# Performance work log

Hardware: AMD Instinct MI355X
Metric: run time of the kernel (lower is better)

## Reference

```python
import jax, jax.numpy as jnp
import numpy as np
import math

B, D, TX, TY = 16, 192, 512, 2048
NEG = -1e9


def _neg_cent(x_mean, x_logs, z):
    # x_mean, x_logs: [B, D, TX]; z: [B, D, TY] -> neg_cent: [B, TY, TX]
    s_p_sq_r = jnp.exp(-2.0 * x_logs)                                   # [B,D,TX]
    nc1 = jnp.sum(-0.5 * math.log(2.0 * math.pi) - x_logs, axis=1, keepdims=True)  # [B,1,TX]
    nc2 = jnp.einsum('bdy,bdx->byx', -0.5 * z * z, s_p_sq_r)            # [B,TY,TX]
    nc3 = jnp.einsum('bdy,bdx->byx', z, x_mean * s_p_sq_r)              # [B,TY,TX]
    nc4 = jnp.sum(-0.5 * x_mean * x_mean * s_p_sq_r, axis=1, keepdims=True)  # [B,1,TX]
    return nc1 + nc2 + nc3 + nc4


def _mas_single(nc):
    # Monotonic alignment search (Viterbi DP) for one sample. nc: [TY, TX]
    ty, tx = nc.shape
    xs = jnp.arange(tx)

    def fwd_step(v_prev, inp):
        nc_row, y = inp
        v_diag = jnp.concatenate([jnp.full((1,), NEG, nc.dtype), v_prev[:-1]])
        take_diag = v_diag > v_prev                                      # bool [TX]
        v = nc_row + jnp.maximum(v_prev, v_diag)
        v = jnp.where(xs <= y, v, NEG)                                   # path cannot be ahead of time
        return v, take_diag

    v0 = jnp.where(xs == 0, nc[0], NEG)
    _, dirs = jax.lax.scan(fwd_step, v0, (nc[1:], jnp.arange(1, ty)))    # dirs: [TY-1, TX]

    def bwd_step(idx, d_row):
        # idx = path position at row y; move to y-1
        new_idx = idx - d_row[idx].astype(idx.dtype)
        return new_idx, idx

    idx0, path_tail = jax.lax.scan(bwd_step, jnp.array(tx - 1, jnp.int32), dirs, reverse=True)
    path = jnp.concatenate([idx0[None], path_tail])                      # [TY]
    return jax.nn.one_hot(path, tx, dtype=nc.dtype)                      # [TY, TX]


def _forward(x_mean, x_logs, z, logw):
    neg_cent = jax.lax.stop_gradient(_neg_cent(x_mean, x_logs, z))
    attn = jax.lax.stop_gradient(jax.vmap(_mas_single)(neg_cent))        # [B,TY,TX]
    w = jnp.sum(attn, axis=1, keepdims=True)                             # [B,1,TX] durations
    logw_ = jnp.log(w + 1e-6)
    l_length = jnp.sum((logw - logw_) ** 2, axis=(1, 2))                 # [B]
    m_p = jnp.einsum('byx,bdx->bdy', attn, x_mean)                       # [B,D,TY]
    logs_p = jnp.einsum('byx,bdx->bdy', attn, x_logs)                    # [B,D,TY]
    out_main = jnp.concatenate([m_p, logs_p], axis=1)                    # [B,2D,TY]
    return out_main, l_length, attn


def setup_inputs() -> dict:
    key = jax.random.key(0)
    k1, k2, k3, k4 = jax.random.split(key, 4)
    return {
        'x_mean': jax.random.normal(k1, (B, D, TX), jnp.float32),
        'x_logs': jax.random.normal(k2, (B, D, TX), jnp.float32),
        'z': jax.random.normal(k3, (B, D, TY), jnp.float32),
        'logw': jax.random.normal(k4, (B, 1, TX), jnp.float32),
    }


def reference(x_mean, x_logs, z, logw):
    return _forward(x_mean, x_logs, z, logw)
```

## Files before the change

kernel.cpp:

```cpp
#include <hip/hip_runtime.h>
#include <hip/hip_bf16.h>
#include <math.h>

#define B_   16
#define D_   192
#define TX_  512
#define TY_  2048
#define NEGV (-1e9f)



typedef __attribute__((address_space(1))) const float glob_f;
typedef __attribute__((address_space(3))) float       lds_f;

__global__ __launch_bounds__(512) void precomp(const float* __restrict__ xm,
                                               const float* __restrict__ xl,
                                               float* __restrict__ S,
                                               float* __restrict__ MS,
                                               float* __restrict__ Cpart) {
    int b = blockIdx.x;
    int p = blockIdx.y;
    int x = threadIdx.x;
    size_t base = ((size_t)b * D_ + p * 32) * TX_;
    const float* mb = xm + base;
    const float* lb = xl + base;
    float* Sb  = S  + base;
    float* MSb = MS + base;
    float c = 0.f;
    for (int d = 0; d < 32; d++) {
        float lg = lb[d * TX_ + x];
        float mn = mb[d * TX_ + x];
        float s  = expf(-2.f * lg);
        float ms = mn * s;
        Sb[d * TX_ + x]  = s;
        MSb[d * TX_ + x] = ms;
        c += -0.9189385332046727f - lg - 0.5f * mn * mn * s;
    }
    Cpart[(b * 6 + p) * TX_ + x] = c;
}

__global__ __launch_bounds__(256) void gemm_nc(const float* __restrict__ z,
                                               const float* __restrict__ S,
                                               const float* __restrict__ MS,
                                               const float* __restrict__ Cpart,
                                               float* __restrict__ NC) {
    int bx = blockIdx.x;
    int by = blockIdx.y;
    int b  = blockIdx.z;
    int tid = threadIdx.x;
    int tx = tid & 15, ty = tid >> 4;
    __shared__ __align__(16) float Zt[16 * 128];
    __shared__ __align__(16) float St[16 * 128];
    __shared__ __align__(16) float MSt[16 * 128];

    float acc[8][8];
#pragma unroll
    for (int i = 0; i < 8; i++)
#pragma unroll
        for (int j = 0; j < 8; j++) acc[i][j] = 0.f;

    int x0 = bx * 128, y0 = by * 128;
    const float* zb  = z  + (size_t)b * D_ * TY_;
    const float* Sb  = S  + (size_t)b * D_ * TX_;
    const float* MSb = MS + (size_t)b * D_ * TX_;

    for (int k0 = 0; k0 < D_; k0 += 16) {
#pragma unroll
        for (int j = 0; j < 2; j++) {
            int f = tid + j * 256;
            int kk = f >> 5, c = (f & 31) * 4;
            __builtin_amdgcn_global_load_lds((glob_f*)(zb  + (size_t)(k0 + kk) * TY_ + y0 + c),
                                             (lds_f*)(Zt  + f * 4), 16, 0, 0);
            __builtin_amdgcn_global_load_lds((glob_f*)(Sb  + (size_t)(k0 + kk) * TX_ + x0 + c),
                                             (lds_f*)(St  + f * 4), 16, 0, 0);
            __builtin_amdgcn_global_load_lds((glob_f*)(MSb + (size_t)(k0 + kk) * TX_ + x0 + c),
                                             (lds_f*)(MSt + f * 4), 16, 0, 0);
        }
        __syncthreads();

#pragma unroll 2
        for (int kk = 0; kk < 16; kk++) {
            float4 z0 = *(const float4*)&Zt[kk * 128 + ty * 4];
            float4 z1 = *(const float4*)&Zt[kk * 128 + 64 + ty * 4];
            float4 s0 = *(const float4*)&St[kk * 128 + tx * 4];
            float4 s1 = *(const float4*)&St[kk * 128 + 64 + tx * 4];
            float4 m0 = *(const float4*)&MSt[kk * 128 + tx * 4];
            float4 m1 = *(const float4*)&MSt[kk * 128 + 64 + tx * 4];
            float4 u0, u1;
            u0.x = -0.5f * z0.x * z0.x; u0.y = -0.5f * z0.y * z0.y;
            u0.z = -0.5f * z0.z * z0.z; u0.w = -0.5f * z0.w * z0.w;
            u1.x = -0.5f * z1.x * z1.x; u1.y = -0.5f * z1.y * z1.y;
            u1.z = -0.5f * z1.z * z1.z; u1.w = -0.5f * z1.w * z1.w;
            float zz[8] = {z0.x, z0.y, z0.z, z0.w, z1.x, z1.y, z1.z, z1.w};
            float uu[8] = {u0.x, u0.y, u0.z, u0.w, u1.x, u1.y, u1.z, u1.w};
            float ss[8] = {s0.x, s0.y, s0.z, s0.w, s1.x, s1.y, s1.z, s1.w};
            float mm[8] = {m0.x, m0.y, m0.z, m0.w, m1.x, m1.y, m1.z, m1.w};
#pragma unroll
            for (int i = 0; i < 8; i++)
#pragma unroll
                for (int j = 0; j < 8; j++)
                    acc[i][j] += uu[i] * ss[j] + zz[i] * mm[j];
        }
        __syncthreads();
    }

    float cv[8] = {0, 0, 0, 0, 0, 0, 0, 0};
#pragma unroll
    for (int p = 0; p < 6; p++) {
        float4 c0 = *(const float4*)&Cpart[(b * 6 + p) * TX_ + x0 + tx * 4];
        float4 c1 = *(const float4*)&Cpart[(b * 6 + p) * TX_ + x0 + 64 + tx * 4];
        cv[0] += c0.x; cv[1] += c0.y; cv[2] += c0.z; cv[3] += c0.w;
        cv[4] += c1.x; cv[5] += c1.y; cv[6] += c1.z; cv[7] += c1.w;
    }

#pragma unroll
    for (int i = 0; i < 8; i++) {
        int y = y0 + ty * 4 + (i & 3) + 64 * (i >> 2);
        float4 o0, o1;
        o0.x = acc[i][0] + cv[0]; o0.y = acc[i][1] + cv[1];
        o0.z = acc[i][2] + cv[2]; o0.w = acc[i][3] + cv[3];
        o1.x = acc[i][4] + cv[4]; o1.y = acc[i][5] + cv[5];
        o1.z = acc[i][6] + cv[6]; o1.w = acc[i][7] + cv[7];
        *(float4*)&NC[((size_t)b * TY_ + y) * TX_ + x0 + tx * 4]      = o0;
        *(float4*)&NC[((size_t)b * TY_ + y) * TX_ + x0 + 64 + tx * 4] = o1;
    }
}

__global__ __launch_bounds__(128, 1) void mas_forward(const float* __restrict__ NC,
                                                      unsigned char* __restrict__ dirs) {
    int b = blockIdx.x;
    int tid = threadIdx.x;
    int wave = tid >> 6;
    int lane = tid & 63;
    const float* ncb = NC + (size_t)b * TY_ * TX_;

    __shared__ __align__(16) float ring[64][512];
    __shared__ int prod_cnt;
    __shared__ int cons_cnt;
    if (tid == 0) { prod_cnt = 0; cons_cnt = 0; }
    __syncthreads();

    if (wave == 1) {
        for (int k = 0; k < 128; k++) {
            while (k - __hip_atomic_load(&cons_cnt, __ATOMIC_ACQUIRE,
                                         __HIP_MEMORY_SCOPE_WORKGROUP) >= 4)
                __builtin_amdgcn_s_sleep(1);
            int slot0 = (k & 3) * 16;
#pragma unroll
            for (int r = 0; r < 16; r++) {
                int y = 1 + k * 16 + r;
                if (y > 2047) y = 2047;
                const float* g = ncb + (size_t)y * TX_ + lane * 4;
                float* l = &ring[slot0 + r][0];
                __builtin_amdgcn_global_load_lds((glob_f*)g,         (lds_f*)l,         16, 0, 0);
                __builtin_amdgcn_global_load_lds((glob_f*)(g + 256), (lds_f*)(l + 256), 16, 0, 0);
            }
            asm volatile("s_waitcnt vmcnt(0)" ::: "memory");
            if (lane == 0)
                __hip_atomic_store(&prod_cnt, k + 1, __ATOMIC_RELEASE,
                                   __HIP_MEMORY_SCOPE_WORKGROUP);
        }
    } else {
        float v[8];
#pragma unroll
        for (int j = 0; j < 8; j++) v[j] = NEGV;
        if (lane == 0) v[0] = ncb[0];

        unsigned char* db = dirs + (size_t)b * 2048 * 64 + lane;
        float bound = NEGV;

        auto row_step = [&](float4 a, float4 c, int y, bool mask) {
            float ncv[8] = {a.x, a.y, a.z, a.w, c.x, c.y, c.z, c.w};
            float vd0 = (lane == 0) ? NEGV : bound;
            float v6o = v[6], v7o = v[7];
            float v7n = ncv[7] + fmaxf(v7o, v6o);
            if (mask && y < 511 && lane * 8 + 7 > y) v7n = NEGV;
            bound = __shfl_up(v7n, 1);
            unsigned bits = (v6o > v7o) ? 0x80u : 0u;
            float vd = vd0;
#pragma unroll
            for (int j = 0; j < 7; j++) {
                float vp = v[j];
                bits |= (vd > vp) ? (1u << j) : 0u;
                v[j] = ncv[j] + fmaxf(vp, vd);
                vd = vp;
            }
            if (mask && y < 511) {
                int xb = lane * 8;
#pragma unroll
                for (int j = 0; j < 7; j++)
                    if (xb + j > y) v[j] = NEGV;
            }
            v[7] = v7n;
            db[(size_t)(y - 1) * 64] = (unsigned char)bits;
        };

        auto wait_chunk = [&](int k) {
            while (__hip_atomic_load(&prod_cnt, __ATOMIC_ACQUIRE,
                                     __HIP_MEMORY_SCOPE_WORKGROUP) < k + 1)
                __builtin_amdgcn_s_sleep(1);
        };
        auto done_chunk = [&](int k) {
            if (lane == 0)
                __hip_atomic_store(&cons_cnt, k + 1, __ATOMIC_RELEASE,
                                   __HIP_MEMORY_SCOPE_WORKGROUP);
        };

        int y = 1;
        for (int k = 0; k < 32; k++) {
            wait_chunk(k);
            int slot0 = (k & 3) * 16;
#pragma unroll
            for (int r = 0; r < 16; r++) {
                float4 a = *(const float4*)&ring[slot0 + r][lane * 8];
                float4 c = *(const float4*)&ring[slot0 + r][lane * 8 + 4];
                row_step(a, c, y, true);
                y++;
            }
            done_chunk(k);
        }
        for (int k = 32; k < 127; k++) {
            wait_chunk(k);
            int slot0 = (k & 3) * 16;
#pragma unroll
            for (int r = 0; r < 16; r++) {
                float4 a = *(const float4*)&ring[slot0 + r][lane * 8];
                float4 c = *(const float4*)&ring[slot0 + r][lane * 8 + 4];
                row_step(a, c, y, false);
                y++;
            }
            done_chunk(k);
        }
        wait_chunk(127);
        {
            int slot0 = (127 & 3) * 16;
#pragma unroll
            for (int r = 0; r < 15; r++) {
                float4 a = *(const float4*)&ring[slot0 + r][lane * 8];
                float4 c = *(const float4*)&ring[slot0 + r][lane * 8 + 4];
                row_step(a, c, y, false);
                y++;
            }
            done_chunk(127);
        }
    }
}

__global__ __launch_bounds__(64, 1) void mas_backtrack(const unsigned* __restrict__ dirs,
                                                       int* __restrict__ path) {
    int b = blockIdx.x;
    int lane = threadIdx.x;
    const unsigned* db = dirs + (size_t)b * 2048 * 16;
    int idx = TX_ - 1;

    for (int y_hi = 2047; y_hi >= 1; y_hi -= 64) {
        int wb = (idx >> 5) - 2;
        if (wb < 0) wb = 0;
        int base = wb << 5;
        int y = y_hi - lane;
        unsigned w0 = 0, w1 = 0, w2 = 0;
        if (y >= 1) {
            const unsigned* r = db + (size_t)(y - 1) * 16 + wb;
            w0 = r[0]; w1 = r[1]; w2 = r[2];
        }
        int steps = (y_hi < 64) ? y_hi : 64;
        int my_path = 0;
#pragma unroll 8
        for (int t = 0; t < steps; t++) {
            if (lane == t) my_path = idx;
            unsigned u0 = (unsigned)__shfl((int)w0, t);
            unsigned u1 = (unsigned)__shfl((int)w1, t);
            unsigned u2 = (unsigned)__shfl((int)w2, t);
            int off = idx - base;
            unsigned w = (off < 32) ? u0 : ((off < 64) ? u1 : u2);
            idx -= (int)((w >> (off & 31)) & 1u);
        }
        if (lane < steps) path[b * TY_ + (y_hi - lane)] = my_path;
    }
    if (lane == 0) path[b * TY_ + 0] = idx;
}

__global__ __launch_bounds__(512) void durations_ll(const int* __restrict__ path,
                                                    const float* __restrict__ logw,
                                                    float* __restrict__ out_l) {
    int b = blockIdx.x;
    int tid = threadIdx.x;
    __shared__ int wcnt[TX_];
    __shared__ float partial[8];
    wcnt[tid] = 0;
    __syncthreads();
    for (int y = tid; y < TY_; y += 512)
        atomicAdd(&wcnt[path[b * TY_ + y]], 1);
    __syncthreads();
    float t = logw[b * TX_ + tid] - logf((float)wcnt[tid] + 1e-6f);
    float sq = t * t;
#pragma unroll
    for (int off = 32; off > 0; off >>= 1) sq += __shfl_down(sq, off);
    if ((tid & 63) == 0) partial[tid >> 6] = sq;
    __syncthreads();
    if (tid == 0) {
        float s = 0.f;
#pragma unroll
        for (int i = 0; i < 8; i++) s += partial[i];
        out_l[b] = s;
    }
}

__global__ __launch_bounds__(256) void gather_main(const int* __restrict__ path,
                                                   const float* __restrict__ xm,
                                                   const float* __restrict__ xl,
                                                   float* __restrict__ out) {
    int c = blockIdx.x;
    int b = blockIdx.y;
    int tid = threadIdx.x;
    const float* src = (c < D_) ? (xm + ((size_t)b * D_ + c) * TX_)
                                : (xl + ((size_t)b * D_ + (c - D_)) * TX_);
    const int* pb = path + b * TY_;
    float* ob = out + ((size_t)b * 2 * D_ + c) * TY_;
#pragma unroll
    for (int k = 0; k < 8; k++) {
        int y = tid + k * 256;
        ob[y] = src[pb[y]];
    }
}

__global__ __launch_bounds__(128) void write_attn(const int* __restrict__ path,
                                                  float* __restrict__ attn) {
    int blk = blockIdx.x;
    int b = blk >> 11;
    int y = blk & 2047;
    int tid = threadIdx.x;
    int p = path[b * TY_ + y];
    float4 val = make_float4(0.f, 0.f, 0.f, 0.f);
    if ((p >> 2) == tid) {
        int r = p & 3;
        if (r == 0) val.x = 1.f;
        else if (r == 1) val.y = 1.f;
        else if (r == 2) val.z = 1.f;
        else val.w = 1.f;
    }
    ((float4*)attn)[((size_t)blk) * 128 + tid] = val;
}

extern "C" void kernel_launch(void* const* d_in, const int* in_sizes, int n_in,
                              void* d_out, int out_size, void* d_ws, size_t ws_size,
                              hipStream_t stream) {
    const float* x_mean = (const float*)d_in[0];
    const float* x_logs = (const float*)d_in[1];
    const float* z      = (const float*)d_in[2];
    const float* logw   = (const float*)d_in[3];
    float* out = (float*)d_out;

    char* ws = (char*)d_ws;
    float* S            = (float*)(ws + 0);
    float* MS           = (float*)(ws + 6291456);
    float* NC           = (float*)(ws + 12615680);
    unsigned char* dirs = (unsigned char*)(ws + 79724544);
    float* Cpart        = (float*)(ws + 79724544);
    int* path           = (int*)(ws + 81821696);

    float* out_main = out;
    float* out_l    = out + 12582912;
    float* out_attn = out + 12582928;

    precomp<<<dim3(B_, 6), dim3(512), 0, stream>>>(x_mean, x_logs, S, MS, Cpart);
    gemm_nc<<<dim3(4, 16, 16), dim3(256), 0, stream>>>(z, S, MS, Cpart, NC);
    mas_forward<<<dim3(B_), dim3(128), 0, stream>>>(NC, dirs);
    mas_backtrack<<<dim3(B_), dim3(64), 0, stream>>>((const unsigned*)dirs, path);
    durations_ll<<<dim3(B_), dim3(512), 0, stream>>>(path, logw, out_l);
    gather_main<<<dim3(384, 16), dim3(256), 0, stream>>>(path, x_mean, x_logs, out_main);
    write_attn<<<dim3(B_ * TY_), dim3(128), 0, stream>>>(path, out_attn);
}
```

Baseline: 799.1 us.

## Split each lane's DP columns into two interleaved halves to shorten serial chain

In the Viterbi forward pass, each lane now owns two groups of 4 columns, one in the lower half of TX and one in the upper half, instead of 8 contiguous columns. The cross-lane boundary values for both halves come from a single rotated shuffle computed early, and lane 0's upper-half boundary is taken from lane 63's lower-half value. LDS reads become two conflict-free float4 loads per row. Direction bits are repacked with an xor-shuffle so each byte still covers 8 contiguous columns. The aim is to cut the serial dependency per row and let the shuffle overlap with the other column updates, at the cost of an extra shuffle and some bit-packing work.

```diff
diff --git a/kernel.cpp b/kernel.cpp
--- a/kernel.cpp
+++ b/kernel.cpp
@@ -166,33 +166,66 @@
         for (int j = 0; j < 8; j++) v[j] = NEGV;
         if (lane == 0) v[0] = ncb[0];
 
-        unsigned char* db = dirs + (size_t)b * 2048 * 64 + lane;
-        float bound = NEGV;
-
-        auto row_step = [&](float4 a, float4 c, int y, bool mask) {
-            float ncv[8] = {a.x, a.y, a.z, a.w, c.x, c.y, c.z, c.w};
-            float vd0 = (lane == 0) ? NEGV : bound;
-            float v6o = v[6], v7o = v[7];
-            float v7n = ncv[7] + fmaxf(v7o, v6o);
-            if (mask && y < 511 && lane * 8 + 7 > y) v7n = NEGV;
-            bound = __shfl_up(v7n, 1);
-            unsigned bits = (v6o > v7o) ? 0x80u : 0u;
-            float vd = vd0;
-#pragma unroll
-            for (int j = 0; j < 7; j++) {
-                float vp = v[j];
-                bits |= (vd > vp) ? (1u << j) : 0u;
-                v[j] = ncv[j] + fmaxf(vp, vd);
-                vd = vp;
-            }
-            if (mask && y < 511) {
-                int xb = lane * 8;
-#pragma unroll
-                for (int j = 0; j < 7; j++)
-                    if (xb + j > y) v[j] = NEGV;
-            }
-            v[7] = v7n;
-            db[(size_t)(y - 1) * 64] = (unsigned char)bits;
+        unsigned char* db = dirs + (size_t)b * 2048 * 64;
+        int doff = (lane & 1) ? (32 + (lane >> 1)) : (lane >> 1);
+        unsigned char* db2 = db + doff;
+
+        float boundA = NEGV;
+        float boundB = NEGV;
+        int lw = (lane + 63) & 63;
+
+        auto row_step = [&](float4 a, float4 c, int y, bool maskph) {
+            float vdA = (lane == 0) ? NEGV : boundA;
+            float vdB = boundB;
+            float o0 = v[0], o1 = v[1], o2 = v[2], o3 = v[3];
+            float o4 = v[4], o5 = v[5], o6 = v[6], o7 = v[7];
+            float n3 = a.w + fmaxf(o3, o2);
+            float n7 = c.w + fmaxf(o7, o6);
+            if (maskph) {
+                if (y < 255 && lane * 4 + 3 > y) n3 = NEGV;
+                if (y < 511 && lane * 4 + 259 > y) n7 = NEGV;
+            }
+            float sA = __shfl(n3, lw);
+            float sB = __shfl(n7, lw);
+            float n0 = a.x + fmaxf(o0, vdA);
+            float n1 = a.y + fmaxf(o1, o0);
+            float n2 = a.z + fmaxf(o2, o1);
+            float n4 = c.x + fmaxf(o4, vdB);
+            float n5 = c.y + fmaxf(o5, o4);
+            float n6 = c.z + fmaxf(o6, o5);
+            unsigned bits = 0;
+            bits |= (vdA > o0) ? 0x1u : 0u;
+            bits |= (o0 > o1) ? 0x2u : 0u;
+            bits |= (o1 > o2) ? 0x4u : 0u;
+            bits |= (o2 > o3) ? 0x8u : 0u;
+            bits |= (vdB > o4) ? 0x10u : 0u;
+            bits |= (o4 > o5) ? 0x20u : 0u;
+            bits |= (o5 > o6) ? 0x40u : 0u;
+            bits |= (o6 > o7) ? 0x80u : 0u;
+            if (maskph) {
+                int xa = lane * 4;
+                if (y < 255) {
+                    if (xa > y) n0 = NEGV;
+                    if (xa + 1 > y) n1 = NEGV;
+                    if (xa + 2 > y) n2 = NEGV;
+                }
+                int xb = 256 + lane * 4;
+                if (y < 511) {
+                    if (xb > y) n4 = NEGV;
+                    if (xb + 1 > y) n5 = NEGV;
+                    if (xb + 2 > y) n6 = NEGV;
+                }
+            }
+            v[0] = n0; v[1] = n1; v[2] = n2; v[3] = n3;
+            v[4] = n4; v[5] = n5; v[6] = n6; v[7] = n7;
+            boundA = sA;
+            boundB = (lane == 0) ? sA : sB;
+            unsigned pk = (bits & 0xFu) | ((bits & 0xF0u) << 4);
+            unsigned pr = (unsigned)__shfl_xor((int)pk, 1);
+            unsigned lowb  = (pk & 0xFu) | ((pr & 0xFu) << 4);
+            unsigned highb = ((pr >> 8) & 0xFu) | (((pk >> 8) & 0xFu) << 4);
+            unsigned byteval = (lane & 1) ? highb : lowb;
+            db2[(size_t)(y - 1) * 64] = (unsigned char)byteval;
         };
 
         auto wait_chunk = [&](int k) {
@@ -212,8 +245,8 @@
             int slot0 = (k & 3) * 16;
 #pragma unroll
             for (int r = 0; r < 16; r++) {
-                float4 a = *(const float4*)&ring[slot0 + r][lane * 8];
-                float4 c = *(const float4*)&ring[slot0 + r][lane * 8 + 4];
+                float4 a = *(const float4*)&ring[slot0 + r][lane * 4];
+                float4 c = *(const float4*)&ring[slot0 + r][256 + lane * 4];
                 row_step(a, c, y, true);
                 y++;
             }
@@ -224,8 +257,8 @@
             int slot0 = (k & 3) * 16;
 #pragma unroll
             for (int r = 0; r < 16; r++) {
-                float4 a = *(const float4*)&ring[slot0 + r][lane * 8];
-                float4 c = *(const float4*)&ring[slot0 + r][lane * 8 + 4];
+                float4 a = *(const float4*)&ring[slot0 + r][lane * 4];
+                float4 c = *(const float4*)&ring[slot0 + r][256 + lane * 4];
                 row_step(a, c, y, false);
                 y++;
             }
@@ -236,8 +269,8 @@
             int slot0 = (127 & 3) * 16;
 #pragma unroll
             for (int r = 0; r < 15; r++) {
-                float4 a = *(const float4*)&ring[slot0 + r][lane * 8];
-                float4 c = *(const float4*)&ring[slot0 + r][lane * 8 + 4];
+                float4 a = *(const float4*)&ring[slot0 + r][lane * 4];
+                float4 c = *(const float4*)&ring[slot0 + r][256 + lane * 4];
                 row_step(a, c, y, false);
                 y++;
             }
```

New measurement: 862.9 us. 1.08x slower.
